# Kernel tuning notes

Measured on AMD Instinct MI355X. Metric: run time of the kernel, lower is better.

## Reference

```python
import jax, jax.numpy as jnp
import numpy as np

NEG_INF = -1.0e9
LEAKY_SLOPE = 0.2


def setup_inputs() -> dict:
    key = jax.random.key(0)
    k1, k2, k3, k4, k5 = jax.random.split(key, 5)
    B, N, IN, F, H = 4, 2048, 128, 64, 4
    h = jax.random.normal(k1, (B, N, IN), dtype=jnp.float32)
    adj_matrix = jax.random.randint(k2, (B, N, N), 0, 2, dtype=jnp.int32)
    W = jax.random.normal(k3, (IN, F * H), dtype=jnp.float32) * 0.05
    a1 = jax.random.normal(k4, (F,), dtype=jnp.float32) * 0.05
    a2 = jax.random.normal(k5, (F,), dtype=jnp.float32) * 0.05
    return {"h": h, "adj_matrix": adj_matrix, "W": W, "a1": a1, "a2": a2}


def reference(h, adj_matrix, W, a1, a2):
    B, N, _ = h.shape
    F = a1.shape[0]
    H = W.shape[1] // F
    # g: [B, H, N, F]
    g = (h @ W).reshape(B, N, H, F).transpose(0, 2, 1, 3)
    # additive attention split: e[p, q] = leakyrelu(a1 . g_q + a2 . g_p)
    s_dst = jnp.einsum("bhnf,f->bhn", g, a1)  # indexed by q (column)
    s_src = jnp.einsum("bhnf,f->bhn", g, a2)  # indexed by p (row)
    e = s_src[:, :, :, None] + s_dst[:, :, None, :]  # [B,H,N,N]
    e = jnp.where(e >= 0, e, LEAKY_SLOPE * e)
    e = jnp.where(adj_matrix[:, None, :, :] == 0, NEG_INF, e)
    attention = jax.nn.softmax(e, axis=-1)  # [B,H,N,N]
    # dropout omitted (deterministic/eval reference)
    h_prime = jnp.einsum("bhpq,bhqf->bpf", attention, g) / H  # mean over heads
    return h_prime, attention.mean(axis=1)
```

## Files before the change

### kernel.cpp

```cpp
#include <hip/hip_runtime.h>
#include <stdint.h>


typedef unsigned char u8;
typedef unsigned short u16;
typedef unsigned int u32;
typedef unsigned long long u64;

typedef float f32x4 __attribute__((ext_vector_type(4)));
typedef short s16x8 __attribute__((ext_vector_type(8)));
typedef u32 u32x4 __attribute__((ext_vector_type(4)));

#define B_ 4
#define N_ 2048
#define IN_ 128
#define F_ 64
#define H_ 4
#define QS_ 8

__device__ __forceinline__ float bf2f(u16 b) {
    u32 u = ((u32)b) << 16;
    return __builtin_bit_cast(float, u);
}
__device__ __forceinline__ u16 f2bf(float f) {
    u32 u = __builtin_bit_cast(u32, f);
    u += 0x7FFFu + ((u >> 16) & 1u);
    return (u16)(u >> 16);
}

__global__ __launch_bounds__(256) void kd_detect(const u32* __restrict__ hw,
                                                 u32* __restrict__ flag) {
    __shared__ int cnt[4];
    int t = threadIdx.x;
    u32 w = hw[t];
    int e0 = (int)((w >> 7) & 0xFFu);
    int sane = (e0 >= 100 && e0 <= 145) ? 1 : 0;
#pragma unroll
    for (int m = 1; m < 64; m <<= 1) sane += __shfl_xor(sane, m, 64);
    if ((t & 63) == 0) cnt[t >> 6] = sane;
    __syncthreads();
    if (t == 0) {
        int s = cnt[0] + cnt[1] + cnt[2] + cnt[3];
        *flag = (s >= 128) ? 1u : 0u;
    }
}

__device__ __forceinline__ u16 conv_elem(const void* p, int i, u32 isbf) {
    if (isbf) return ((const u16*)p)[i];
    return f2bf(((const float*)p)[i]);
}
__global__ __launch_bounds__(256) void kc_convert(
    const void* __restrict__ h, const void* __restrict__ W, const void* __restrict__ a1,
    const void* __restrict__ a2, const u32* __restrict__ flag, u16* __restrict__ hc,
    u16* __restrict__ wt, u16* __restrict__ a1c, u16* __restrict__ a2c) {
    u32 isbf = *flag;
    int idx = blockIdx.x * 256 + threadIdx.x;
    const int NH = B_ * N_ * IN_;
    if (idx < NH) {
        hc[idx] = conv_elem(h, idx, isbf);
        return;
    }
    int j = idx - NH;
    if (j < IN_ * 256) {
        int k = j >> 8, c = j & 255;
        wt[c * IN_ + k] = conv_elem(W, j, isbf);
        return;
    }
    j -= IN_ * 256;
    if (j < F_) {
        a1c[j] = conv_elem(a1, j, isbf);
        return;
    }
    j -= F_;
    if (j < F_) a2c[j] = conv_elem(a2, j, isbf);
}

__global__ __launch_bounds__(256) void k1_proj(
    const u16* __restrict__ h, const u16* __restrict__ Wt,
    const u16* __restrict__ a1, const u16* __restrict__ a2,
    u16* __restrict__ g_t, u16* __restrict__ sdb, u32* __restrict__ e2pn,
    float* __restrict__ ssA, float2* __restrict__ ssE) {
    int b = blockIdx.x >> 7;
    int n0 = (blockIdx.x & 127) * 16;
    int w = threadIdx.x >> 6;
    int lane = threadIdx.x & 63;
    int quad = lane >> 4, l15 = lane & 15;

    f32x4 acc[4];
#pragma unroll
    for (int i = 0; i < 4; i++) acc[i] = 0.0f;

    s16x8 A[4];
#pragma unroll
    for (int kt = 0; kt < 4; kt++) {
        const s16x8* ap =
            (const s16x8*)(h + ((size_t)(b * N_ + n0 + l15) * IN_ + kt * 32 + quad * 8));
        A[kt] = *ap;
    }
#pragma unroll
    for (int kt = 0; kt < 4; kt++) {
#pragma unroll
        for (int ft = 0; ft < 4; ft++) {
            int c = w * 64 + ft * 16 + l15;
            const s16x8* bp = (const s16x8*)(Wt + ((size_t)c * IN_ + kt * 32 + quad * 8));
            acc[ft] = __builtin_amdgcn_mfma_f32_16x16x32_bf16(A[kt], *bp, acc[ft], 0, 0, 0);
        }
    }
    __shared__ float ct[4][64][20];
#pragma unroll
    for (int ft = 0; ft < 4; ft++)
#pragma unroll
        for (int r = 0; r < 4; r++) ct[w][ft * 16 + l15][quad * 4 + r] = acc[ft][r];
    __syncthreads();

    float v[16];
#pragma unroll
    for (int n = 0; n < 16; n++) v[n] = ct[w][lane][n];

    {
        u16 tmp[16];
#pragma unroll
        for (int n = 0; n < 16; n++) tmp[n] = f2bf(v[n]);
        size_t base = ((size_t)((b * H_ + w) * F_ + lane)) * N_ + n0;
        s16x8 t0, t1;
#pragma unroll
        for (int n = 0; n < 8; n++) { t0[n] = (short)tmp[n]; t1[n] = (short)tmp[n + 8]; }
        *(s16x8*)(g_t + base) = t0;
        *(s16x8*)(g_t + base + 8) = t1;
    }
    float a1v = bf2f(a1[lane]);
    float a2v = bf2f(a2[lane]);
    float sdv = 0.f, ssv = 0.f;
#pragma unroll
    for (int n = 0; n < 16; n++) {
        float x = v[n] * a1v;
        float y = v[n] * a2v;
#pragma unroll
        for (int m = 1; m < 64; m <<= 1) {
            x += __shfl_xor(x, m, 64);
            y += __shfl_xor(y, m, 64);
        }
        if (lane == n) { sdv = x; ssv = y; }
    }
    if (lane < 16) {
        size_t o = (size_t)(b * H_ + w) * N_ + n0 + lane;
        sdb[o] = f2bf(sdv);
        float e2p = __expf(sdv), e2n = __expf(0.2f * sdv);
        e2pn[o] = (((u32)f2bf(e2p)) << 16) | (u32)f2bf(e2n);
        ssA[o] = ssv;
        ssE[o] = make_float2(__expf(ssv), __expf(0.2f * ssv));
    }
}

__global__ __launch_bounds__(256) void k2a_rowsum(
    const int* __restrict__ adj, const u16* __restrict__ sdb, const u32* __restrict__ e2pn,
    const float* __restrict__ ssA, const float2* __restrict__ ssE,
    float2* __restrict__ E1, u32* __restrict__ pk32) {
    int b = blockIdx.x >> 9;
    int p0 = (blockIdx.x & 511) * 4;
    int t = threadIdx.x;
    int w = t >> 6, lane = t & 63;

    __shared__ u8 nib[4][512];

    float tau[4][4];
#pragma unroll
    for (int r = 0; r < 4; r++)
#pragma unroll
        for (int hh = 0; hh < 4; hh++)
            tau[r][hh] = -ssA[(size_t)(b * H_ + hh) * N_ + p0 + r];

    float S[32];
#pragma unroll
    for (int i = 0; i < 32; i++) S[i] = 0.f;

#pragma unroll
    for (int i = 0; i < 2; i++) {
        int qi = i * 256 + t;
        int q = qi * 4;
        float af[4][4];
#pragma unroll
        for (int r = 0; r < 4; r++) {
            int4 av = *(const int4*)(adj + (size_t)(b * N_ + p0 + r) * N_ + q);
            af[r][0] = (av.x != 0) ? 1.f : 0.f;
            af[r][1] = (av.y != 0) ? 1.f : 0.f;
            af[r][2] = (av.z != 0) ? 1.f : 0.f;
            af[r][3] = (av.w != 0) ? 1.f : 0.f;
            u32 nb = (av.x != 0 ? 1u : 0u) | (av.y != 0 ? 2u : 0u) |
                     (av.z != 0 ? 4u : 0u) | (av.w != 0 ? 8u : 0u);
            nib[r][qi] = (u8)nb;
        }
#pragma unroll
        for (int hh = 0; hh < 4; hh++) {
            size_t o = (size_t)(b * H_ + hh) * N_ + q;
            u64 sd4 = *(const u64*)(sdb + o);
            u32x4 pn4 = *(const u32x4*)(e2pn + o);
            float sdf[4], e2p[4], e2n[4];
#pragma unroll
            for (int j = 0; j < 4; j++) {
                sdf[j] = bf2f((u16)(sd4 >> (16 * j)));
                e2p[j] = __builtin_bit_cast(float, pn4[j] & 0xFFFF0000u);
                e2n[j] = __builtin_bit_cast(float, pn4[j] << 16);
            }
#pragma unroll
            for (int r = 0; r < 4; r++) {
#pragma unroll
                for (int j = 0; j < 4; j++) {
                    bool ge = sdf[j] >= tau[r][hh];
                    S[(r * 4 + hh) * 2 + 0] += ge ? af[r][j] * e2p[j] : 0.f;
                    S[(r * 4 + hh) * 2 + 1] += ge ? 0.f : af[r][j] * e2n[j];
                }
            }
        }
    }
    __syncthreads();
    {
        int r = t >> 6, m8 = t & 63;
        u64 nn = *(const u64*)&nib[r][m8 * 8];
        u32 wd = 0;
#pragma unroll
        for (int d = 0; d < 4; d++) {
            u32 lo = (u32)(nn >> (16 * d)) & 0xFu;
            u32 hi = (u32)(nn >> (16 * d + 8)) & 0xFu;
            wd |= (lo | (hi << 4)) << (8 * d);
        }
        pk32[(size_t)(b * N_ + p0 + r) * 64 + m8] = wd;
    }
#pragma unroll
    for (int k = 0; k < 32; k++) {
        float x = S[k];
#pragma unroll
        for (int m = 1; m < 64; m <<= 1) x += __shfl_xor(x, m, 64);
        S[k] = x;
    }
    __shared__ float sred[4][32];
    if (lane == 0) {
#pragma unroll
        for (int k = 0; k < 32; k++) sred[w][k] = S[k];
    }
    __syncthreads();
    if (t < 16) {
        int r = t >> 2, hh = t & 3;
        float sp = 0.f, sn = 0.f;
#pragma unroll
        for (int ww = 0; ww < 4; ww++) {
            sp += sred[ww][t * 2];
            sn += sred[ww][t * 2 + 1];
        }
        size_t o = (size_t)(b * H_ + hh) * N_ + p0 + r;
        float2 se = ssE[o];
        float l = se.x * sp + se.y * sn;
        float inv = (l > 0.f) ? 0.25f / l : 0.f;
        E1[o] = make_float2(se.x * inv, se.y * inv);
    }
}

__global__ __launch_bounds__(64) void k2b_attn(
    const u16* __restrict__ sdb, const u32* __restrict__ e2pn, const float* __restrict__ ssA,
    const float2* __restrict__ E1, const u32* __restrict__ pk32,
    const u16* __restrict__ g_t, const u32* __restrict__ flag, void* __restrict__ d_out_v,
    u16* __restrict__ part) {
    int bid = blockIdx.x;
    int s = bid & (QS_ - 1);
    int pt = (bid >> 3) & 127;
    int b = bid >> 10;
    int qb = s * (N_ / QS_);
    int lane = threadIdx.x;
    int quad = lane >> 4, l15 = lane & 15;
    int p0 = pt * 16;
    int row = p0 + l15;
    u32 isbf = *flag;

    __shared__ __align__(16) u16 lsd[4][256];
    __shared__ __align__(16) u32 le2[4][256];
#pragma unroll
    for (int hh = 0; hh < 4; hh++) {
        size_t o = (size_t)(b * H_ + hh) * N_ + qb + lane * 4;
        *(u64*)&lsd[hh][lane * 4] = *(const u64*)(sdb + o);
        *(u32x4*)&le2[hh][lane * 4] = *(const u32x4*)(e2pn + o);
    }
    __syncthreads();

    float E1p[4], E1n[4], tau[4];
#pragma unroll
    for (int hh = 0; hh < 4; hh++) {
        size_t o = (size_t)(b * H_ + hh) * N_ + row;
        float2 e1 = E1[o];
        E1p[hh] = e1.x;
        E1n[hh] = e1.y;
        tau[hh] = -ssA[o];
    }
    f32x4 acc[4][4];
#pragma unroll
    for (int i = 0; i < 4; i++)
#pragma unroll
        for (int j = 0; j < 4; j++) acc[i][j] = 0.0f;

    const u32* pkrow = pk32 + (size_t)(b * N_ + row) * 64 + (qb >> 5);
    size_t am_base = ((size_t)(b * N_ + row)) * N_ + qb + quad * 8;
    u16* amb = (u16*)d_out_v + (size_t)B_ * N_ * F_;
    float* amf = (float*)d_out_v + (size_t)B_ * N_ * F_;

#pragma unroll 1
    for (int c = 0; c < 8; c++) {
        int qq = c * 32 + quad * 8;
        u32 awd = pkrow[c];
        u32 byte_ = (awd >> (quad * 8)) & 0xFFu;
        float bitf[8];
#pragma unroll
        for (int j = 0; j < 8; j++) bitf[j] = ((byte_ >> j) & 1u) ? 1.0f : 0.0f;

        float amv[8];
#pragma unroll
        for (int j = 0; j < 8; j++) amv[j] = 0.f;

#pragma unroll
        for (int hh = 0; hh < 4; hh++) {
            s16x8 sd8 = *(const s16x8*)&lsd[hh][qq];
            u32x4 e2a = *(const u32x4*)&le2[hh][qq];
            u32x4 e2b = *(const u32x4*)&le2[hh][qq + 4];
            float wv[8];
#pragma unroll
            for (int j = 0; j < 8; j++) {
                float sdf = bf2f((u16)sd8[j]);
                bool ge = sdf >= tau[hh];
                u32 pn = (j < 4) ? e2a[j] : e2b[j - 4];
                float e2 = ge ? __builtin_bit_cast(float, pn & 0xFFFF0000u)
                              : __builtin_bit_cast(float, pn << 16);
                float e1v = ge ? E1p[hh] : E1n[hh];
                float ww = e1v * e2 * bitf[j];
                wv[j] = ww;
                amv[j] += ww;
            }
            s16x8 af;
#pragma unroll
            for (int j = 0; j < 8; j++) af[j] = (short)f2bf(wv[j]);
#pragma unroll
            for (int ft = 0; ft < 4; ft++) {
                const s16x8* bp =
                    (const s16x8*)(g_t + (size_t)((b * H_ + hh) * F_ + ft * 16 + l15) * N_ +
                                   qb + c * 32 + quad * 8);
                acc[hh][ft] = __builtin_amdgcn_mfma_f32_16x16x32_bf16(af, *bp, acc[hh][ft], 0, 0, 0);
            }
        }
        if (isbf) {
            s16x8 amp;
#pragma unroll
            for (int j = 0; j < 8; j++) amp[j] = (short)f2bf(amv[j]);
            *(s16x8*)(amb + am_base + c * 32) = amp;
        } else {
            f32x4 lo, hi;
#pragma unroll
            for (int j = 0; j < 4; j++) { lo[j] = amv[j]; hi[j] = amv[j + 4]; }
            *(f32x4*)(amf + am_base + c * 32) = lo;
            *(f32x4*)(amf + am_base + c * 32 + 4) = hi;
        }
    }
#pragma unroll
    for (int ft = 0; ft < 4; ft++) {
#pragma unroll
        for (int r = 0; r < 4; r++) {
            float sum = acc[0][ft][r] + acc[1][ft][r] + acc[2][ft][r] + acc[3][ft][r];
            int pout = p0 + quad * 4 + r;
            int f = ft * 16 + l15;
            part[(size_t)((s * B_ + b) * N_ + pout) * F_ + f] = f2bf(sum);
        }
    }
}

__global__ __launch_bounds__(256) void k3_reduce(const u16* __restrict__ part,
                                                 const u32* __restrict__ flag,
                                                 void* __restrict__ out) {
    int idx = blockIdx.x * 256 + threadIdx.x;
    float s = 0.f;
#pragma unroll
    for (int i = 0; i < QS_; i++) s += bf2f(part[(size_t)i * (B_ * N_ * F_) + idx]);
    if (*flag)
        ((u16*)out)[idx] = f2bf(s);
    else
        ((float*)out)[idx] = s;
}

extern "C" void kernel_launch(void* const* d_in, const int* in_sizes, int n_in,
                              void* d_out, int out_size, void* d_ws, size_t ws_size,
                              hipStream_t stream) {
    const void* h = d_in[0];
    const int* adj = (const int*)d_in[1];
    const void* W = d_in[2];
    const void* a1 = d_in[3];
    const void* a2 = d_in[4];

    char* ws = (char*)d_ws;
    u32* flag = (u32*)(ws + 0);
    u16* a1c = (u16*)(ws + 64);
    u16* a2c = (u16*)(ws + 192);
    u16* wt = (u16*)(ws + 1024);
    u16* hc = (u16*)(ws + 66560);
    u16* g_t = (u16*)(ws + 2163712);
    u16* sdb = (u16*)(ws + 6358016);
    u32* e2pn = (u32*)(ws + 6423552);
    float* ssA = (float*)(ws + 6554624);
    float2* ssE = (float2*)(ws + 6685696);
    float2* E1 = (float2*)(ws + 6947840);
    u32* pk = (u32*)(ws + 7209984);
    u16* part = (u16*)(ws + 9307136);

    kd_detect<<<1, 256, 0, stream>>>((const u32*)h, flag);
    kc_convert<<<(B_ * N_ * IN_ + IN_ * 256 + 2 * F_ + 255) / 256, 256, 0, stream>>>(
        h, W, a1, a2, flag, hc, wt, a1c, a2c);
    k1_proj<<<512, 256, 0, stream>>>(hc, wt, a1c, a2c, g_t, sdb, e2pn, ssA, ssE);
    k2a_rowsum<<<2048, 256, 0, stream>>>(adj, sdb, e2pn, ssA, ssE, E1, pk);
    k2b_attn<<<4096, 64, 0, stream>>>(sdb, e2pn, ssA, E1, (const u32*)pk, g_t, flag,
                                      d_out, part);
    k3_reduce<<<2048, 256, 0, stream>>>(part, flag, d_out);
}
```

Measured before the change: 218.3 us.

## Store g in fragment-major layout and software-prefetch MFMA B operands

The projection kernel now writes g in a fragment-contiguous layout, so each lane's 8-element MFMA B fragment sits in one contiguous 16-byte slot and a wave reads 1KB contiguously per fragment. The attention kernel double-buffers these B fragments, loading the next (chunk, head) step while computing the current one, and preloads the packed adjacency words up front. Heads now accumulate into a single set of accumulators, cutting accumulator registers fourfold and dropping the final cross-head sum. The aim is to hide global-load latency and make B loads coalesced, at the cost of extra live registers for the prefetch buffers.

```diff
diff --git a/kernel.cpp b/kernel.cpp
--- a/kernel.cpp
+++ b/kernel.cpp
@@ -78,7 +78,7 @@
 __global__ __launch_bounds__(256) void k1_proj(
     const u16* __restrict__ h, const u16* __restrict__ Wt,
     const u16* __restrict__ a1, const u16* __restrict__ a2,
-    u16* __restrict__ g_t, u16* __restrict__ sdb, u32* __restrict__ e2pn,
+    u16* __restrict__ g_f, u16* __restrict__ sdb, u32* __restrict__ e2pn,
     float* __restrict__ ssA, float2* __restrict__ ssE) {
     int b = blockIdx.x >> 7;
     int n0 = (blockIdx.x & 127) * 16;
@@ -118,15 +118,20 @@
     for (int n = 0; n < 16; n++) v[n] = ct[w][lane][n];
 
     {
-        u16 tmp[16];
-#pragma unroll
-        for (int n = 0; n < 16; n++) tmp[n] = f2bf(v[n]);
-        size_t base = ((size_t)((b * H_ + w) * F_ + lane)) * N_ + n0;
-        s16x8 t0, t1;
-#pragma unroll
-        for (int n = 0; n < 8; n++) { t0[n] = (short)tmp[n]; t1[n] = (short)tmp[n + 8]; }
-        *(s16x8*)(g_t + base) = t0;
-        *(s16x8*)(g_t + base + 8) = t1;
+        int chunk = n0 >> 5;
+        int gq0 = (n0 >> 3) & 2;
+#pragma unroll
+        for (int p = 0; p < 2; p++) {
+            int ft = p * 2 + (lane >> 5);
+            int lq = (lane >> 4) & 1;
+            int fl = lane & 15;
+            s16x8 tv;
+#pragma unroll
+            for (int j = 0; j < 8; j++) tv[j] = (short)f2bf(ct[w][ft * 16 + fl][lq * 8 + j]);
+            size_t off =
+                ((size_t)(((b * H_ + w) * 4 + ft) * 64 + chunk) * 64 + (gq0 + lq) * 16 + fl) * 8;
+            *(s16x8*)(g_f + off) = tv;
+        }
     }
     float a1v = bf2f(a1[lane]);
     float a2v = bf2f(a2[lane]);
@@ -258,7 +263,7 @@
 __global__ __launch_bounds__(64) void k2b_attn(
     const u16* __restrict__ sdb, const u32* __restrict__ e2pn, const float* __restrict__ ssA,
     const float2* __restrict__ E1, const u32* __restrict__ pk32,
-    const u16* __restrict__ g_t, const u32* __restrict__ flag, void* __restrict__ d_out_v,
+    const u16* __restrict__ g_f, const u32* __restrict__ flag, void* __restrict__ d_out_v,
     u16* __restrict__ part) {
     int bid = blockIdx.x;
     int s = bid & (QS_ - 1);
@@ -290,13 +295,22 @@
         E1n[hh] = e1.y;
         tau[hh] = -ssA[o];
     }
-    f32x4 acc[4][4];
-#pragma unroll
-    for (int i = 0; i < 4; i++)
-#pragma unroll
-        for (int j = 0; j < 4; j++) acc[i][j] = 0.0f;
+    f32x4 acc[4];
+#pragma unroll
+    for (int i = 0; i < 4; i++) acc[i] = 0.0f;
 
     const u32* pkrow = pk32 + (size_t)(b * N_ + row) * 64 + (qb >> 5);
+    u32 pkw[8];
+#pragma unroll
+    for (int c = 0; c < 8; c++) pkw[c] = pkrow[c];
+
+    const size_t hstride = (size_t)4 * 64 * 512;
+    const u16* gb = g_f + (size_t)b * H_ * hstride + (size_t)(qb >> 5) * 512 + lane * 8;
+
+    s16x8 Bc[4], Bn[4];
+#pragma unroll
+    for (int ft = 0; ft < 4; ft++) Bc[ft] = *(const s16x8*)(gb + (size_t)ft * 32768);
+
     size_t am_base = ((size_t)(b * N_ + row)) * N_ + qb + quad * 8;
     u16* amb = (u16*)d_out_v + (size_t)B_ * N_ * F_;
     float* amf = (float*)d_out_v + (size_t)B_ * N_ * F_;
@@ -304,8 +318,7 @@
 #pragma unroll 1
     for (int c = 0; c < 8; c++) {
         int qq = c * 32 + quad * 8;
-        u32 awd = pkrow[c];
-        u32 byte_ = (awd >> (quad * 8)) & 0xFFu;
+        u32 byte_ = (pkw[c] >> (quad * 8)) & 0xFFu;
         float bitf[8];
 #pragma unroll
         for (int j = 0; j < 8; j++) bitf[j] = ((byte_ >> j) & 1u) ? 1.0f : 0.0f;
@@ -316,6 +329,14 @@
 
 #pragma unroll
         for (int hh = 0; hh < 4; hh++) {
+            {
+                int idx = (c * 4 + hh + 1) & 31;
+                int c2 = idx >> 2, h2 = idx & 3;
+#pragma unroll
+                for (int ft = 0; ft < 4; ft++)
+                    Bn[ft] = *(const s16x8*)(gb + (size_t)h2 * hstride + (size_t)ft * 32768 +
+                                             (size_t)c2 * 512);
+            }
             s16x8 sd8 = *(const s16x8*)&lsd[hh][qq];
             u32x4 e2a = *(const u32x4*)&le2[hh][qq];
             u32x4 e2b = *(const u32x4*)&le2[hh][qq + 4];
@@ -336,12 +357,10 @@
 #pragma unroll
             for (int j = 0; j < 8; j++) af[j] = (short)f2bf(wv[j]);
 #pragma unroll
-            for (int ft = 0; ft < 4; ft++) {
-                const s16x8* bp =
-                    (const s16x8*)(g_t + (size_t)((b * H_ + hh) * F_ + ft * 16 + l15) * N_ +
-                                   qb + c * 32 + quad * 8);
-                acc[hh][ft] = __builtin_amdgcn_mfma_f32_16x16x32_bf16(af, *bp, acc[hh][ft], 0, 0, 0);
-            }
+            for (int ft = 0; ft < 4; ft++)
+                acc[ft] = __builtin_amdgcn_mfma_f32_16x16x32_bf16(af, Bc[ft], acc[ft], 0, 0, 0);
+#pragma unroll
+            for (int ft = 0; ft < 4; ft++) Bc[ft] = Bn[ft];
         }
         if (isbf) {
             s16x8 amp;
@@ -360,10 +379,9 @@
     for (int ft = 0; ft < 4; ft++) {
 #pragma unroll
         for (int r = 0; r < 4; r++) {
-            float sum = acc[0][ft][r] + acc[1][ft][r] + acc[2][ft][r] + acc[3][ft][r];
             int pout = p0 + quad * 4 + r;
             int f = ft * 16 + l15;
-            part[(size_t)((s * B_ + b) * N_ + pout) * F_ + f] = f2bf(sum);
+            part[(size_t)((s * B_ + b) * N_ + pout) * F_ + f] = f2bf(acc[ft][r]);
         }
     }
 }
@@ -396,7 +414,7 @@
     u16* a2c = (u16*)(ws + 192);
     u16* wt = (u16*)(ws + 1024);
     u16* hc = (u16*)(ws + 66560);
-    u16* g_t = (u16*)(ws + 2163712);
+    u16* g_f = (u16*)(ws + 2163712);
     u16* sdb = (u16*)(ws + 6358016);
     u32* e2pn = (u32*)(ws + 6423552);
     float* ssA = (float*)(ws + 6554624);
@@ -408,9 +426,9 @@
     kd_detect<<<1, 256, 0, stream>>>((const u32*)h, flag);
     kc_convert<<<(B_ * N_ * IN_ + IN_ * 256 + 2 * F_ + 255) / 256, 256, 0, stream>>>(
         h, W, a1, a2, flag, hc, wt, a1c, a2c);
-    k1_proj<<<512, 256, 0, stream>>>(hc, wt, a1c, a2c, g_t, sdb, e2pn, ssA, ssE);
+    k1_proj<<<512, 256, 0, stream>>>(hc, wt, a1c, a2c, g_f, sdb, e2pn, ssA, ssE);
     k2a_rowsum<<<2048, 256, 0, stream>>>(adj, sdb, e2pn, ssA, ssE, E1, pk);
-    k2b_attn<<<4096, 64, 0, stream>>>(sdb, e2pn, ssA, E1, (const u32*)pk, g_t, flag,
+    k2b_attn<<<4096, 64, 0, stream>>>(sdb, e2pn, ssA, E1, (const u32*)pk, g_f, flag,
                                       d_out, part);
     k3_reduce<<<2048, 256, 0, stream>>>(part, flag, d_out);
 }
```

Result: faster. 191.8 us (-12.1%).
